# Optimization experiments

Measured on AMD Instinct MI355X. Metric: run time of the kernel, lower is better.

Reference implementation:

```python
import jax, jax.numpy as jnp
import numpy as np

SEQ, NSTEPS = 8192, 2048
IDIM, HDIM, NL = 256, 1024, 4


def setup_inputs() -> dict:
    key = jax.random.key(0)
    ks = jax.random.split(key, 6)
    s = 0.02  # small init so tanh recurrence stays well-conditioned
    return {
        "xs": jax.random.normal(ks[0], (SEQ, IDIM), dtype=jnp.float32),
        "Wx0": jax.random.normal(ks[1], (IDIM, HDIM), dtype=jnp.float32) * s,
        "Wh0": jax.random.normal(ks[2], (HDIM, HDIM), dtype=jnp.float32) * s,
        "b0": jnp.zeros((HDIM,), dtype=jnp.float32),
        "Wx_rest": jax.random.normal(ks[3], (NL - 1, HDIM, HDIM), dtype=jnp.float32) * s,
        "Wh_rest": jax.random.normal(ks[4], (NL - 1, HDIM, HDIM), dtype=jnp.float32) * s,
        "b_rest": jnp.zeros((NL - 1, HDIM), dtype=jnp.float32),
        "out_W": jax.random.normal(ks[5], (IDIM, HDIM), dtype=jnp.float32) * s,  # eqx Linear: (out, in)
        "out_b": jnp.zeros((IDIM,), dtype=jnp.float32),
        "n_steps": NSTEPS,
    }


def _layer_scan(xs, Wx, Wh, b):
    # open-loop scan of one tanh RNN cell over the whole sequence
    pre = xs @ Wx + b  # (T, H): hoist input projection out of the scan

    def step(h, p):
        h = jnp.tanh(p + h @ Wh)
        return h, h

    h0 = jnp.zeros((Wh.shape[0],), dtype=xs.dtype)
    last, outs = jax.lax.scan(step, h0, pre)
    return last, outs


def reference(xs, Wx0, Wh0, b0, Wx_rest, Wh_rest, b_rest, out_W, out_b, n_steps):
    # open_loop: run each layer's scan over the full sequence
    states = []
    h, seq = _layer_scan(xs, Wx0, Wh0, b0)
    states.append(h)
    for i in range(Wx_rest.shape[0]):
        h, seq = _layer_scan(seq, Wx_rest[i], Wh_rest[i], b_rest[i])
        states.append(h)
    ol_outs = seq @ out_W.T + out_b  # (T, IDIM) vmap'd out_layer

    def ar_step(carry, _):
        sts, x = carry
        new_sts = []
        h = jnp.tanh(x @ Wx0 + sts[0] @ Wh0 + b0)
        new_sts.append(h)
        x = h
        for i in range(Wx_rest.shape[0]):
            h = jnp.tanh(x @ Wx_rest[i] + sts[i + 1] @ Wh_rest[i] + b_rest[i])
            new_sts.append(h)
            x = h
        x = out_W @ x + out_b
        return (tuple(new_sts), x), x

    carry = (tuple(states), ol_outs[-1])
    _, ar_outs = jax.lax.scan(ar_step, carry, None, length=n_steps)
    return jnp.concatenate([ol_outs, ar_outs], axis=0)  # (T + n_steps, IDIM)
```

## Files before the change

### kernel.cpp

```cpp
#include <hip/hip_runtime.h>
#include <math.h>

#define SEQ    8192
#define NSTEPS 2048
#define NTOT   (SEQ + NSTEPS)
#define IDIM   256
#define HDIM   1024

#define NWG    128
#define TPB    512
#define WPB    8
#define RD     8

typedef unsigned long long u64;

#define WT_FLOATS   (8ull*HDIM*HDIM)
#define BF_FLOAT    WT_FLOATS
#define RING_FLOAT  (WT_FLOATS + HDIM)
#define RING_U64S   (4ull*RD*HDIM)
#define PROG_FLOAT  (RING_FLOAT + 2ull*RING_U64S)


__global__ void k_fuse_w(const float* __restrict__ outW, const float* __restrict__ Wx0,
                         float* __restrict__ ws) {
    int l = blockIdx.x * 256 + threadIdx.x;
    int j = blockIdx.y;
    float acc = 0.f;
    for (int k = 0; k < IDIM; ++k)
        acc += outW[(size_t)k * HDIM + l] * Wx0[(size_t)k * HDIM + j];
    ws[(size_t)j * HDIM + l] = acc;
}

__global__ void k_fuse_b(const float* __restrict__ b0, const float* __restrict__ outb,
                         const float* __restrict__ Wx0, float* __restrict__ ws) {
    int j = blockIdx.x * 256 + threadIdx.x;
    float acc = b0[j];
    for (int k = 0; k < IDIM; ++k)
        acc += outb[k] * Wx0[(size_t)k * HDIM + j];
    ws[BF_FLOAT + j] = acc;
}

__global__ void k_pack(const float* __restrict__ Wh0, const float* __restrict__ Wxr,
                       const float* __restrict__ Whr, float* __restrict__ ws) {
    __shared__ float t[32][33];
    int z = blockIdx.z;
    const float* src; int slot;
    if (z == 0)      { src = Wh0;                                  slot = 1; }
    else if (z <= 3) { src = Wxr + (size_t)(z - 1) * HDIM * HDIM;  slot = 2 * z; }
    else             { src = Whr + (size_t)(z - 4) * HDIM * HDIM;  slot = 2 * (z - 4) + 3; }
    int j0 = blockIdx.x * 32, l0 = blockIdx.y * 32;
    t[threadIdx.y][threadIdx.x] = src[(size_t)(l0 + threadIdx.y) * HDIM + j0 + threadIdx.x];
    __syncthreads();
    float* dst = ws + (size_t)slot * HDIM * HDIM;
    dst[(size_t)(j0 + threadIdx.y) * HDIM + (l0 + threadIdx.x)] = t[threadIdx.x][threadIdx.y];
}

__global__ void k_init(float* __restrict__ ws) {
    int t = blockIdx.x * blockDim.x + threadIdx.x;
    ((u64*)(ws + RING_FLOAT))[t] = 0ull;
    if (t < NWG) ((unsigned*)(ws + PROG_FLOAT))[t] = 0u;
}


__device__ __forceinline__ float wsum(float v) {
#pragma unroll
    for (int off = 32; off > 0; off >>= 1) v += __shfl_xor(v, off, 64);
    return v;
}

__device__ __forceinline__ float ftanh(float x) {
    x = fminf(15.f, fmaxf(-15.f, x));
    float e = __builtin_amdgcn_exp2f(x * 2.8853900817779268f);
    return (e - 1.f) * __builtin_amdgcn_rcpf(e + 1.f);
}

__device__ __forceinline__ void capture8(const u64* slot, unsigned want,
                                         float* dst, int lane, int kbase) {
    unsigned done = 0;
    for (;;) {
        u64 v[8];
#pragma unroll
        for (int k = 0; k < 8; ++k) {
            v[k] = 0;
            if (!(done & (1u << k)))
                v[k] = __hip_atomic_load(slot + lane + 64 * (kbase + k),
                                         __ATOMIC_RELAXED, __HIP_MEMORY_SCOPE_AGENT);
        }
#pragma unroll
        for (int k = 0; k < 8; ++k) {
            if (!(done & (1u << k)) && ((unsigned)(v[k] >> 32) == want)) {
                dst[lane + 64 * (kbase + k)] = __uint_as_float((unsigned)v[k]);
                done |= 1u << k;
            }
        }
        if (__all(done == 0xFFu)) return;
    }
}

__global__ __launch_bounds__(TPB, 1) void k_scan(
    const float* __restrict__ xs, const float* __restrict__ Wx0,
    const float* __restrict__ b0, const float* __restrict__ brest,
    const float* __restrict__ outW, const float* __restrict__ outb,
    float* __restrict__ ws, float* __restrict__ out)
{
    const int lane  = threadIdx.x & 63;
    const int wv    = threadIdx.x >> 6;
    const int layer = blockIdx.x >> 5;
    const int wgl   = blockIdx.x & 31;
    const int jw    = wgl * WPB + wv;
    const int j0    = jw * 4;

    __shared__ float ldsOwn[2][HDIM];
    __shared__ float ldsUp[2][HDIM];

    u64* ring = (u64*)(ws + RING_FLOAT);
    unsigned* prog = (unsigned*)(ws + PROG_FLOAT);
    const int cons = (layer + 1) & 3;

    float A[4][16], B[4][16];
#pragma unroll
    for (int c = 0; c < 4; ++c)
#pragma unroll
        for (int k = 0; k < 16; ++k) {
            A[c][k] = ws[((size_t)(2 * layer) * HDIM + (j0 + c)) * HDIM + lane + 64 * k];
            B[c][k] = ws[((size_t)(2 * layer + 1) * HDIM + (j0 + c)) * HDIM + lane + 64 * k];
        }
    float wx0[4][4];
    if (layer == 0) {
#pragma unroll
        for (int c = 0; c < 4; ++c)
#pragma unroll
            for (int k = 0; k < 4; ++k)
                wx0[c][k] = Wx0[(size_t)(lane + 64 * k) * HDIM + (j0 + c)];
    }
    float ow[16]; float obv = 0.f;
    if (layer == 3) {
#pragma unroll
        for (int k = 0; k < 16; ++k) ow[k] = outW[(size_t)jw * HDIM + lane + 64 * k];
        obv = outb[jw];
    }
    float bb[4], bfc[4];
#pragma unroll
    for (int c = 0; c < 4; ++c) {
        bb[c]  = (layer == 0) ? b0[j0 + c] : brest[(size_t)(layer - 1) * HDIM + j0 + c];
        bfc[c] = (layer == 0) ? ws[BF_FLOAT + j0 + c] : 0.f;
    }

    int minp = 0;

    for (int n = 1; n <= NTOT; ++n) {
        const int par = n & 1;
        const bool xphase = (layer == 0) && (n <= SEQ);

        if (minp < n - 7) {
            for (;;) {
                unsigned pv = __hip_atomic_load(&prog[cons * 32 + (lane & 31)],
                                                __ATOMIC_RELAXED, __HIP_MEMORY_SCOPE_AGENT);
#pragma unroll
                for (int off = 32; off > 0; off >>= 1) {
                    unsigned o = (unsigned)__shfl_xor((int)pv, off, 64);
                    pv = pv < o ? pv : o;
                }
                minp = (int)pv;
                if (minp >= n - 7) break;
                __builtin_amdgcn_s_sleep(2);
            }
        }

        float xv[4];
        if (xphase) {
            const float* xr = xs + (size_t)(n - 1) * IDIM;
#pragma unroll
            for (int k = 0; k < 4; ++k) xv[k] = xr[lane + 64 * k];
        }

        if (wv < 2) {
            capture8(ring + ((size_t)layer * RD + ((n - 1) & (RD - 1))) * HDIM,
                     (unsigned)(n - 1), ldsOwn[par], lane, wv * 8);
        } else if (wv < 4 && !xphase) {
            const int ul = (layer == 0) ? 3 : layer - 1;
            const unsigned want = (layer == 0) ? (unsigned)(n - 1) : (unsigned)n;
            capture8(ring + ((size_t)ul * RD + (want & (RD - 1))) * HDIM,
                     want, ldsUp[par], lane, (wv - 2) * 8);
        }
        __syncthreads();
        if (threadIdx.x == 0)
            __hip_atomic_store(&prog[blockIdx.x], (unsigned)n, __ATOMIC_RELAXED, __HIP_MEMORY_SCOPE_AGENT);

        float a0 = 0.f, a1 = 0.f, a2 = 0.f, a3 = 0.f;
        if (xphase) {
#pragma unroll
            for (int k = 0; k < 4; ++k) {
                float x = xv[k];
                a0 += x * wx0[0][k]; a1 += x * wx0[1][k]; a2 += x * wx0[2][k]; a3 += x * wx0[3][k];
            }
        } else {
#pragma unroll
            for (int k = 0; k < 16; ++k) {
                float x = ldsUp[par][lane + 64 * k];
                a0 += x * A[0][k]; a1 += x * A[1][k]; a2 += x * A[2][k]; a3 += x * A[3][k];
            }
        }
#pragma unroll
        for (int k = 0; k < 16; ++k) {
            float y = ldsOwn[par][lane + 64 * k];
            a0 += y * B[0][k]; a1 += y * B[1][k]; a2 += y * B[2][k]; a3 += y * B[3][k];
        }
        a0 = wsum(a0); a1 = wsum(a1); a2 = wsum(a2); a3 = wsum(a3);
        const bool fph = (layer == 0) && (n > SEQ);
        float r0 = ftanh(a0 + (fph ? bfc[0] : bb[0]));
        float r1 = ftanh(a1 + (fph ? bfc[1] : bb[1]));
        float r2 = ftanh(a2 + (fph ? bfc[2] : bb[2]));
        float r3 = ftanh(a3 + (fph ? bfc[3] : bb[3]));

        {
            u64* dst = ring + ((size_t)layer * RD + (n & (RD - 1))) * HDIM + j0;
            if (lane < 4) {
                float v = (lane == 0) ? r0 : (lane == 1) ? r1 : (lane == 2) ? r2 : r3;
                __hip_atomic_store(dst + lane,
                                   ((u64)(unsigned)n << 32) | (u64)__float_as_uint(v),
                                   __ATOMIC_RELAXED, __HIP_MEMORY_SCOPE_AGENT);
            }
        }

        if (layer == 3 && n >= 2) {
            float a = 0.f;
#pragma unroll
            for (int k = 0; k < 16; ++k) a += ldsOwn[par][lane + 64 * k] * ow[k];
            a = wsum(a);
            if (lane == 0) out[(size_t)(n - 2) * IDIM + jw] = a + obv;
        }
    }

    if (layer == 3) {
        if (wv < 2)
            capture8(ring + ((size_t)3 * RD + (NTOT & (RD - 1))) * HDIM,
                     (unsigned)NTOT, ldsOwn[0], lane, wv * 8);
        __syncthreads();
        float a = 0.f;
#pragma unroll
        for (int k = 0; k < 16; ++k) a += ldsOwn[0][lane + 64 * k] * ow[k];
        a = wsum(a);
        if (lane == 0) out[(size_t)(NTOT - 1) * IDIM + jw] = a + obv;
    }
}


extern "C" void kernel_launch(void* const* d_in, const int* in_sizes, int n_in,
                              void* d_out, int out_size, void* d_ws, size_t ws_size,
                              hipStream_t stream) {
    (void)in_sizes; (void)n_in; (void)out_size; (void)ws_size;
    const float* xs   = (const float*)d_in[0];
    const float* Wx0  = (const float*)d_in[1];
    const float* Wh0  = (const float*)d_in[2];
    const float* b0   = (const float*)d_in[3];
    const float* Wxr  = (const float*)d_in[4];
    const float* Whr  = (const float*)d_in[5];
    const float* brst = (const float*)d_in[6];
    const float* outW = (const float*)d_in[7];
    const float* outb = (const float*)d_in[8];
    float* ws  = (float*)d_ws;
    float* out = (float*)d_out;

    k_fuse_w<<<dim3(4, HDIM), dim3(256), 0, stream>>>(outW, Wx0, ws);
    k_fuse_b<<<dim3(4), dim3(256), 0, stream>>>(b0, outb, Wx0, ws);
    k_pack<<<dim3(32, 32, 7), dim3(32, 32), 0, stream>>>(Wh0, Wxr, Whr, ws);
    k_init<<<dim3(64), dim3(512), 0, stream>>>(ws);

    void* args[] = { (void*)&xs, (void*)&Wx0, (void*)&b0, (void*)&brst,
                     (void*)&outW, (void*)&outb, (void*)&ws, (void*)&out };
    hipError_t e = hipLaunchCooperativeKernel((void*)k_scan, dim3(NWG), dim3(TPB),
                                              args, 0, stream);
    if (e != hipSuccess) {
        k_scan<<<dim3(NWG), dim3(TPB), 0, stream>>>(xs, Wx0, b0, brst, outW, outb, ws, out);
    }
}
```

Baseline: 49.94 ms.

## Replace per-step block barrier with LDS flags and deepen cross-layer ring

Removes the per-step __syncthreads in the persistent scan kernel. Waves now signal each other through workgroup-scope LDS flags and per-wave completion counters, so compute waves start as soon as the buffer they need is captured. In the closed-loop phase the own-state dot product runs before the upstream capture, overlapping the wait on the previous layer with useful work. The ring depth grows from 8 to 32 with a matching producer credit, letting layers drift further apart, and the init kernel launch grows to cover the larger ring. This adds spin-wait traffic on LDS and memory-ordering risk in exchange for less lockstep stalling.

```diff
diff --git a/kernel.cpp b/kernel.cpp
--- a/kernel.cpp
+++ b/kernel.cpp
@@ -10,7 +10,8 @@
 #define NWG    128
 #define TPB    512
 #define WPB    8
-#define RD     8
+#define RD     32
+#define CREDIT (RD - 8)
 
 typedef unsigned long long u64;
 
@@ -97,6 +98,24 @@
     }
 }
 
+__device__ __forceinline__ void ldsGuard(int* ld, int n, int lane) {
+    for (;;) {
+        int m = __hip_atomic_load(&ld[lane & 7], __ATOMIC_RELAXED, __HIP_MEMORY_SCOPE_WORKGROUP);
+        int o = __shfl_xor(m, 1, 64); m = o < m ? o : m;
+        o = __shfl_xor(m, 2, 64);     m = o < m ? o : m;
+        o = __shfl_xor(m, 4, 64);     m = o < m ? o : m;
+        if (m >= n - 2) return;
+    }
+}
+
+__device__ __forceinline__ void waitFlag(unsigned* f, unsigned n) {
+    for (;;) {
+        unsigned x = __hip_atomic_load(&f[0], __ATOMIC_ACQUIRE, __HIP_MEMORY_SCOPE_WORKGROUP);
+        unsigned y = __hip_atomic_load(&f[1], __ATOMIC_ACQUIRE, __HIP_MEMORY_SCOPE_WORKGROUP);
+        if (x == n && y == n) return;
+    }
+}
+
 __global__ __launch_bounds__(TPB, 1) void k_scan(
     const float* __restrict__ xs, const float* __restrict__ Wx0,
     const float* __restrict__ b0, const float* __restrict__ brest,
@@ -112,11 +131,20 @@
 
     __shared__ float ldsOwn[2][HDIM];
     __shared__ float ldsUp[2][HDIM];
+    __shared__ unsigned fOwn[2][2];
+    __shared__ unsigned fUp[2][2];
+    __shared__ int lastDone[WPB];
 
     u64* ring = (u64*)(ws + RING_FLOAT);
     unsigned* prog = (unsigned*)(ws + PROG_FLOAT);
     const int cons = (layer + 1) & 3;
 
+    if (threadIdx.x < 2) {
+        fOwn[threadIdx.x][0] = 0; fOwn[threadIdx.x][1] = 0;
+        fUp[threadIdx.x][0]  = 0; fUp[threadIdx.x][1]  = 0;
+    }
+    if (threadIdx.x < WPB) lastDone[threadIdx.x] = 0;
+
     float A[4][16], B[4][16];
 #pragma unroll
     for (int c = 0; c < 4; ++c)
@@ -146,13 +174,16 @@
         bfc[c] = (layer == 0) ? ws[BF_FLOAT + j0 + c] : 0.f;
     }
 
+    __syncthreads();
+
     int minp = 0;
 
     for (int n = 1; n <= NTOT; ++n) {
         const int par = n & 1;
         const bool xphase = (layer == 0) && (n <= SEQ);
-
-        if (minp < n - 7) {
+        const bool upLate = (n > SEQ);
+
+        if (minp < n - CREDIT) {
             for (;;) {
                 unsigned pv = __hip_atomic_load(&prog[cons * 32 + (lane & 31)],
                                                 __ATOMIC_RELAXED, __HIP_MEMORY_SCOPE_AGENT);
@@ -162,7 +193,7 @@
                     pv = pv < o ? pv : o;
                 }
                 minp = (int)pv;
-                if (minp >= n - 7) break;
+                if (minp >= n - CREDIT) break;
                 __builtin_amdgcn_s_sleep(2);
             }
         }
@@ -174,38 +205,71 @@
             for (int k = 0; k < 4; ++k) xv[k] = xr[lane + 64 * k];
         }
 
-        if (wv < 2) {
+        const bool isOwnCap = (wv < 2);
+        const bool isUpCap  = (wv >= 2 && wv < 4 && !xphase);
+        const int  ul       = (layer == 0) ? 3 : layer - 1;
+        const unsigned want = (layer == 0) ? (unsigned)(n - 1) : (unsigned)n;
+
+        if (isOwnCap) {
+            ldsGuard(lastDone, n, lane);
             capture8(ring + ((size_t)layer * RD + ((n - 1) & (RD - 1))) * HDIM,
                      (unsigned)(n - 1), ldsOwn[par], lane, wv * 8);
-        } else if (wv < 4 && !xphase) {
-            const int ul = (layer == 0) ? 3 : layer - 1;
-            const unsigned want = (layer == 0) ? (unsigned)(n - 1) : (unsigned)n;
+            if (lane == 0)
+                __hip_atomic_store(&fOwn[par][wv], (unsigned)n,
+                                   __ATOMIC_RELEASE, __HIP_MEMORY_SCOPE_WORKGROUP);
+        }
+        if (isUpCap && !upLate) {
+            ldsGuard(lastDone, n, lane);
             capture8(ring + ((size_t)ul * RD + (want & (RD - 1))) * HDIM,
                      want, ldsUp[par], lane, (wv - 2) * 8);
-        }
-        __syncthreads();
-        if (threadIdx.x == 0)
-            __hip_atomic_store(&prog[blockIdx.x], (unsigned)n, __ATOMIC_RELAXED, __HIP_MEMORY_SCOPE_AGENT);
+            if (lane == 0)
+                __hip_atomic_store(&fUp[par][wv - 2], (unsigned)n,
+                                   __ATOMIC_RELEASE, __HIP_MEMORY_SCOPE_WORKGROUP);
+        }
 
         float a0 = 0.f, a1 = 0.f, a2 = 0.f, a3 = 0.f;
+
+#define A_PART_X() do { _Pragma("unroll")                                          \
+        for (int k = 0; k < 4; ++k) { float x = xv[k];                             \
+            a0 += x * wx0[0][k]; a1 += x * wx0[1][k];                              \
+            a2 += x * wx0[2][k]; a3 += x * wx0[3][k]; } } while (0)
+#define A_PART() do { _Pragma("unroll")                                            \
+        for (int k = 0; k < 16; ++k) { float x = ldsUp[par][lane + 64 * k];        \
+            a0 += x * A[0][k]; a1 += x * A[1][k];                                  \
+            a2 += x * A[2][k]; a3 += x * A[3][k]; } } while (0)
+#define B_PART() do { _Pragma("unroll")                                            \
+        for (int k = 0; k < 16; ++k) { float y = ldsOwn[par][lane + 64 * k];       \
+            a0 += y * B[0][k]; a1 += y * B[1][k];                                  \
+            a2 += y * B[2][k]; a3 += y * B[3][k]; } } while (0)
+
         if (xphase) {
-#pragma unroll
-            for (int k = 0; k < 4; ++k) {
-                float x = xv[k];
-                a0 += x * wx0[0][k]; a1 += x * wx0[1][k]; a2 += x * wx0[2][k]; a3 += x * wx0[3][k];
+            A_PART_X();
+            waitFlag(&fOwn[par][0], (unsigned)n);
+            B_PART();
+        } else if (!upLate) {
+            waitFlag(&fUp[par][0], (unsigned)n);
+            A_PART();
+            waitFlag(&fOwn[par][0], (unsigned)n);
+            B_PART();
+        } else {
+            waitFlag(&fOwn[par][0], (unsigned)n);
+            B_PART();
+            if (isUpCap) {
+                ldsGuard(lastDone, n, lane);
+                capture8(ring + ((size_t)ul * RD + (want & (RD - 1))) * HDIM,
+                         want, ldsUp[par], lane, (wv - 2) * 8);
+                if (lane == 0)
+                    __hip_atomic_store(&fUp[par][wv - 2], (unsigned)n,
+                                       __ATOMIC_RELEASE, __HIP_MEMORY_SCOPE_WORKGROUP);
             }
-        } else {
-#pragma unroll
-            for (int k = 0; k < 16; ++k) {
-                float x = ldsUp[par][lane + 64 * k];
-                a0 += x * A[0][k]; a1 += x * A[1][k]; a2 += x * A[2][k]; a3 += x * A[3][k];
-            }
-        }
-#pragma unroll
-        for (int k = 0; k < 16; ++k) {
-            float y = ldsOwn[par][lane + 64 * k];
-            a0 += y * B[0][k]; a1 += y * B[1][k]; a2 += y * B[2][k]; a3 += y * B[3][k];
-        }
+            waitFlag(&fUp[par][0], (unsigned)n);
+            A_PART();
+        }
+
+        if (wv == 7 && lane == 0)
+            __hip_atomic_store(&prog[blockIdx.x], (unsigned)n,
+                               __ATOMIC_RELAXED, __HIP_MEMORY_SCOPE_AGENT);
+
         a0 = wsum(a0); a1 = wsum(a1); a2 = wsum(a2); a3 = wsum(a3);
         const bool fph = (layer == 0) && (n > SEQ);
         float r0 = ftanh(a0 + (fph ? bfc[0] : bb[0]));
@@ -230,19 +294,30 @@
             a = wsum(a);
             if (lane == 0) out[(size_t)(n - 2) * IDIM + jw] = a + obv;
         }
+
+        __hip_atomic_store(&lastDone[wv], n, __ATOMIC_RELEASE, __HIP_MEMORY_SCOPE_WORKGROUP);
     }
 
     if (layer == 3) {
-        if (wv < 2)
+        const int par2 = (NTOT + 1) & 1;
+        if (wv < 2) {
+            ldsGuard(lastDone, NTOT + 1, lane);
             capture8(ring + ((size_t)3 * RD + (NTOT & (RD - 1))) * HDIM,
-                     (unsigned)NTOT, ldsOwn[0], lane, wv * 8);
-        __syncthreads();
+                     (unsigned)NTOT, ldsOwn[par2], lane, wv * 8);
+            if (lane == 0)
+                __hip_atomic_store(&fOwn[par2][wv], (unsigned)(NTOT + 1),
+                                   __ATOMIC_RELEASE, __HIP_MEMORY_SCOPE_WORKGROUP);
+        }
+        waitFlag(&fOwn[par2][0], (unsigned)(NTOT + 1));
         float a = 0.f;
 #pragma unroll
-        for (int k = 0; k < 16; ++k) a += ldsOwn[0][lane + 64 * k] * ow[k];
+        for (int k = 0; k < 16; ++k) a += ldsOwn[par2][lane + 64 * k] * ow[k];
         a = wsum(a);
         if (lane == 0) out[(size_t)(NTOT - 1) * IDIM + jw] = a + obv;
     }
+#undef A_PART_X
+#undef A_PART
+#undef B_PART
 }
 
 
@@ -265,7 +340,7 @@
     k_fuse_w<<<dim3(4, HDIM), dim3(256), 0, stream>>>(outW, Wx0, ws);
     k_fuse_b<<<dim3(4), dim3(256), 0, stream>>>(b0, outb, Wx0, ws);
     k_pack<<<dim3(32, 32, 7), dim3(32, 32), 0, stream>>>(Wh0, Wxr, Whr, ws);
-    k_init<<<dim3(64), dim3(512), 0, stream>>>(ws);
+    k_init<<<dim3(256), dim3(512), 0, stream>>>(ws);
 
     void* args[] = { (void*)&xs, (void*)&Wx0, (void*)&b0, (void*)&brst,
                      (void*)&outW, (void*)&outb, (void*)&ws, (void*)&out };
```

Result: slower. 91.50 ms (+83.2%).

## Deepen ring buffer and move flow-control polling to a dedicated wave

Applied to the files above, without the earlier changes.

Enlarges the inter-layer ring from 8 to 32 slots, which allows up to 24 steps of producer run-ahead before back-pressure. Back-pressure polling of consumer progress moves to a single wave: it prefetches progress counters each step and publishes the minimum through shared memory, and the other waves only read that LDS value. The next step's xs row is also prefetched into registers during the current step. This aims to cut agent-scope polling latency and stalls on the recurrence critical path, at the cost of a larger ring footprint that k_init must clear.

```diff
diff --git a/kernel.cpp b/kernel.cpp
--- a/kernel.cpp
+++ b/kernel.cpp
@@ -10,7 +10,8 @@
 #define NWG    128
 #define TPB    512
 #define WPB    8
-#define RD     8
+#define RD     32
+#define CREDIT (RD - 8)
 
 typedef unsigned long long u64;
 
@@ -68,6 +69,15 @@
     return v;
 }
 
+__device__ __forceinline__ int wmin(int v) {
+#pragma unroll
+    for (int off = 32; off > 0; off >>= 1) {
+        int o = __shfl_xor(v, off, 64);
+        v = o < v ? o : v;
+    }
+    return v;
+}
+
 __device__ __forceinline__ float ftanh(float x) {
     x = fminf(15.f, fmaxf(-15.f, x));
     float e = __builtin_amdgcn_exp2f(x * 2.8853900817779268f);
@@ -112,11 +122,14 @@
 
     __shared__ float ldsOwn[2][HDIM];
     __shared__ float ldsUp[2][HDIM];
+    __shared__ int   ldsMinp;
 
     u64* ring = (u64*)(ws + RING_FLOAT);
     unsigned* prog = (unsigned*)(ws + PROG_FLOAT);
     const int cons = (layer + 1) & 3;
 
+    if (threadIdx.x == 0) ldsMinp = 0;
+
     float A[4][16], B[4][16];
 #pragma unroll
     for (int c = 0; c < 4; ++c)
@@ -146,32 +159,39 @@
         bfc[c] = (layer == 0) ? ws[BF_FLOAT + j0 + c] : 0.f;
     }
 
-    int minp = 0;
+    float xv[4] = {0.f, 0.f, 0.f, 0.f}, xp[4] = {0.f, 0.f, 0.f, 0.f};
+    if (layer == 0) {
+#pragma unroll
+        for (int k = 0; k < 4; ++k) xv[k] = xs[lane + 64 * k];
+    }
+
+    unsigned pvReg = 0;
+
+    __syncthreads();
 
     for (int n = 1; n <= NTOT; ++n) {
         const int par = n & 1;
         const bool xphase = (layer == 0) && (n <= SEQ);
 
-        if (minp < n - 7) {
-            for (;;) {
-                unsigned pv = __hip_atomic_load(&prog[cons * 32 + (lane & 31)],
-                                                __ATOMIC_RELAXED, __HIP_MEMORY_SCOPE_AGENT);
-#pragma unroll
-                for (int off = 32; off > 0; off >>= 1) {
-                    unsigned o = (unsigned)__shfl_xor((int)pv, off, 64);
-                    pv = pv < o ? pv : o;
-                }
-                minp = (int)pv;
-                if (minp >= n - 7) break;
+        if (wv == 5) {
+            int m = wmin((int)pvReg);
+            if (lane == 0)
+                __hip_atomic_store(&ldsMinp, m, __ATOMIC_RELAXED, __HIP_MEMORY_SCOPE_WORKGROUP);
+            while (m < n - CREDIT) {
                 __builtin_amdgcn_s_sleep(2);
-            }
-        }
-
-        float xv[4];
-        if (xphase) {
-            const float* xr = xs + (size_t)(n - 1) * IDIM;
-#pragma unroll
-            for (int k = 0; k < 4; ++k) xv[k] = xr[lane + 64 * k];
+                unsigned p = __hip_atomic_load(&prog[cons * 32 + (lane & 31)],
+                                               __ATOMIC_RELAXED, __HIP_MEMORY_SCOPE_AGENT);
+                m = wmin((int)p);
+                if (lane == 0)
+                    __hip_atomic_store(&ldsMinp, m, __ATOMIC_RELAXED, __HIP_MEMORY_SCOPE_WORKGROUP);
+            }
+        } else {
+            if (__hip_atomic_load(&ldsMinp, __ATOMIC_RELAXED, __HIP_MEMORY_SCOPE_WORKGROUP)
+                < n - CREDIT) {
+                do { __builtin_amdgcn_s_sleep(2); }
+                while (__hip_atomic_load(&ldsMinp, __ATOMIC_RELAXED, __HIP_MEMORY_SCOPE_WORKGROUP)
+                       < n - CREDIT);
+            }
         }
 
         if (wv < 2) {
@@ -187,6 +207,15 @@
         if (threadIdx.x == 0)
             __hip_atomic_store(&prog[blockIdx.x], (unsigned)n, __ATOMIC_RELAXED, __HIP_MEMORY_SCOPE_AGENT);
 
+        if (xphase && n < SEQ) {
+            const float* xr = xs + (size_t)n * IDIM;
+#pragma unroll
+            for (int k = 0; k < 4; ++k) xp[k] = xr[lane + 64 * k];
+        }
+        if (wv == 5)
+            pvReg = __hip_atomic_load(&prog[cons * 32 + (lane & 31)],
+                                      __ATOMIC_RELAXED, __HIP_MEMORY_SCOPE_AGENT);
+
         float a0 = 0.f, a1 = 0.f, a2 = 0.f, a3 = 0.f;
         if (xphase) {
 #pragma unroll
@@ -229,6 +258,11 @@
             for (int k = 0; k < 16; ++k) a += ldsOwn[par][lane + 64 * k] * ow[k];
             a = wsum(a);
             if (lane == 0) out[(size_t)(n - 2) * IDIM + jw] = a + obv;
+        }
+
+        if (xphase && n < SEQ) {
+#pragma unroll
+            for (int k = 0; k < 4; ++k) xv[k] = xp[k];
         }
     }
 
@@ -265,7 +299,7 @@
     k_fuse_w<<<dim3(4, HDIM), dim3(256), 0, stream>>>(outW, Wx0, ws);
     k_fuse_b<<<dim3(4), dim3(256), 0, stream>>>(b0, outb, Wx0, ws);
     k_pack<<<dim3(32, 32, 7), dim3(32, 32), 0, stream>>>(Wh0, Wxr, Whr, ws);
-    k_init<<<dim3(64), dim3(512), 0, stream>>>(ws);
+    k_init<<<dim3(256), dim3(512), 0, stream>>>(ws);
 
     void* args[] = { (void*)&xs, (void*)&Wx0, (void*)&b0, (void*)&brst,
                      (void*)&outW, (void*)&outb, (void*)&ws, (void*)&out };
```

Result: no change. 50.55 ms (+1.2%).
